# Kernel tuning notes

Hardware: AMD Instinct MI355X
Metric: run time of the kernel (lower is better)

## Reference

```python
import jax, jax.numpy as jnp
import numpy as np

def setup_inputs() -> dict:
    key = jax.random.key(0)
    x = jax.random.normal(key, (4096, 3, 64, 64), dtype=jnp.float32)
    return {"x": x}

def reference(x):
    # x: [N, C=3, H, W]; attention runs over the N dim with feature dim H*W
    N, C, H, W = x.shape
    out = x.reshape(N, C, H * W)          # [N, 3, HW]
    q, k, v = out[:, 0], out[:, 1], out[:, 2]  # each [N, HW]
    dp = (q @ k.T) * 0.5                  # [N, N]
    attn = jax.nn.softmax(dp, axis=-1)
    # dropout omitted (eval-mode / deterministic reference)
    return attn @ v                       # [N, HW]
```

## Files before the change

### kernel.cpp

```cpp
#include <hip/hip_runtime.h>
#include <hip/hip_bf16.h>
#include <cstdint>

#define N 4096
#define ROWSTRIDE 12288

typedef __attribute__((ext_vector_type(8))) _Float16 half8;
typedef __attribute__((ext_vector_type(4))) _Float16 half4v;
typedef __attribute__((ext_vector_type(4))) float floatx4;

__global__ __launch_bounds__(256) void pack_qk(const float* __restrict__ x,
                                               _Float16* __restrict__ qh,
                                               _Float16* __restrict__ kh) {
    const size_t tid = (size_t)blockIdx.x * 256 + threadIdx.x;
    const int i  = (int)(tid >> 10);
    const int c4 = (int)(tid & 1023);
    const float4* xr = (const float4*)(x + (size_t)i * ROWSTRIDE);
    float4 q = xr[c4];
    float4 k = xr[1024 + c4];
    half4v qo = {(_Float16)(q.x * 0.5f), (_Float16)(q.y * 0.5f),
                 (_Float16)(q.z * 0.5f), (_Float16)(q.w * 0.5f)};
    half4v ko = {(_Float16)k.x, (_Float16)k.y, (_Float16)k.z, (_Float16)k.w};
    *(half4v*)(qh + tid * 4) = qo;
    *(half4v*)(kh + tid * 4) = ko;
}

__global__ __launch_bounds__(256) void transpose_v(const float* __restrict__ x,
                                                   _Float16* __restrict__ vt) {
    __shared__ float tile[32][33];
    const int j0 = blockIdx.x * 32;
    const int d0 = blockIdx.y * 32;
    const int t  = threadIdx.x;
    const int r  = t >> 3;
    const int c4 = t & 7;
    const float4 val = *(const float4*)(x + (size_t)(j0 + r) * ROWSTRIDE + 8192 + d0 + c4 * 4);
    tile[r][c4 * 4 + 0] = val.x;
    tile[r][c4 * 4 + 1] = val.y;
    tile[r][c4 * 4 + 2] = val.z;
    tile[r][c4 * 4 + 3] = val.w;
    __syncthreads();
    half4v o = {(_Float16)tile[c4 * 4 + 0][r], (_Float16)tile[c4 * 4 + 1][r],
                (_Float16)tile[c4 * 4 + 2][r], (_Float16)tile[c4 * 4 + 3][r]};
    *(half4v*)(vt + (size_t)(d0 + r) * N + j0 + c4 * 4) = o;
}

#define GL2LDS(g, l)                                                                     \
    __builtin_amdgcn_global_load_lds((const __attribute__((address_space(1))) void*)(g), \
                                     (__attribute__((address_space(3))) void*)(l), 16, 0, 0)

__global__ __launch_bounds__(256) void gemm_nt(const _Float16* __restrict__ A,
                                               const _Float16* __restrict__ Bt,
                                               float* __restrict__ C) {
    __shared__ _Float16 As[2 * 128 * 32];
    __shared__ _Float16 Bs[2 * 128 * 32];
    const int t    = threadIdx.x;
    const int wave = t >> 6;
    const int lane = t & 63;
    const int wr   = wave >> 1, wc = wave & 1;
    const int rowBase = blockIdx.y * 128;
    const int colBase = blockIdx.x * 128;

    floatx4 acc[4][4] = {};

    const int ldRow = t >> 2;
    const int ldCol = (t & 3) * 8;
    const _Float16* ga0 = A  + (size_t)(rowBase + ldRow) * N + ldCol;
    const _Float16* gb0 = Bt + (size_t)(colBase + ldRow) * N + ldCol;
    _Float16* lA = &As[wave * 512];
    _Float16* lB = &Bs[wave * 512];

    const int fr = lane & 15;
    const int fk = (lane >> 4) * 8;

    for (int kt = 0; kt < 64; ++kt) {
        const int k0 = kt * 64;
        __syncthreads();
        GL2LDS(ga0 + k0, lA);
        GL2LDS(ga0 + k0 + (size_t)64 * N, lA + 2048);
        GL2LDS(gb0 + k0, lB);
        GL2LDS(gb0 + k0 + (size_t)64 * N, lB + 2048);
        GL2LDS(ga0 + k0 + 32, lA + 4096);
        GL2LDS(ga0 + k0 + 32 + (size_t)64 * N, lA + 6144);
        GL2LDS(gb0 + k0 + 32, lB + 4096);
        GL2LDS(gb0 + k0 + 32 + (size_t)64 * N, lB + 6144);
        __syncthreads();

#pragma unroll
        for (int ks = 0; ks < 2; ++ks) {
            half8 af[4], bf[4];
#pragma unroll
            for (int mt = 0; mt < 4; ++mt)
                af[mt] = *(half8*)&As[ks * 4096 + (wr * 64 + mt * 16 + fr) * 32 + fk];
#pragma unroll
            for (int nt = 0; nt < 4; ++nt)
                bf[nt] = *(half8*)&Bs[ks * 4096 + (wc * 64 + nt * 16 + fr) * 32 + fk];
#pragma unroll
            for (int mt = 0; mt < 4; ++mt)
#pragma unroll
                for (int nt = 0; nt < 4; ++nt)
                    acc[mt][nt] = __builtin_amdgcn_mfma_f32_16x16x32_f16(af[mt], bf[nt],
                                                                         acc[mt][nt], 0, 0, 0);
        }
    }

    const int quad = lane >> 4;
#pragma unroll
    for (int mt = 0; mt < 4; ++mt) {
#pragma unroll
        for (int nt = 0; nt < 4; ++nt) {
#pragma unroll
            for (int r = 0; r < 4; ++r) {
                const int row = rowBase + wr * 64 + mt * 16 + quad * 4 + r;
                const int col = colBase + wc * 64 + nt * 16 + fr;
                C[(size_t)row * N + col] = acc[mt][nt][r];
            }
        }
    }
}

__global__ __launch_bounds__(256) void softmax_rows(const float* __restrict__ S,
                                                    _Float16* __restrict__ P) {
    const int row = blockIdx.x;
    const int t   = threadIdx.x;
    const float4* Sr = (const float4*)(S + (size_t)row * N);

    float4 v[4];
    float lmax = -3.0e38f;
#pragma unroll
    for (int r = 0; r < 4; ++r) {
        v[r] = Sr[t + 256 * r];
        lmax = fmaxf(lmax, fmaxf(fmaxf(v[r].x, v[r].y), fmaxf(v[r].z, v[r].w)));
    }
#pragma unroll
    for (int off = 32; off; off >>= 1) lmax = fmaxf(lmax, __shfl_xor(lmax, off, 64));
    __shared__ float redm[4], reds[4];
    const int wave = t >> 6, lane = t & 63;
    if (lane == 0) redm[wave] = lmax;
    __syncthreads();
    const float m = fmaxf(fmaxf(redm[0], redm[1]), fmaxf(redm[2], redm[3]));

    float lsum = 0.f;
#pragma unroll
    for (int r = 0; r < 4; ++r) {
        v[r].x = __expf(v[r].x - m);
        v[r].y = __expf(v[r].y - m);
        v[r].z = __expf(v[r].z - m);
        v[r].w = __expf(v[r].w - m);
        lsum += (v[r].x + v[r].y) + (v[r].z + v[r].w);
    }
#pragma unroll
    for (int off = 32; off; off >>= 1) lsum += __shfl_xor(lsum, off, 64);
    if (lane == 0) reds[wave] = lsum;
    __syncthreads();
    const float inv = 1.0f / (((reds[0] + reds[1]) + (reds[2] + reds[3])));

#pragma unroll
    for (int r = 0; r < 4; ++r) {
        half4v o = {(_Float16)(v[r].x * inv), (_Float16)(v[r].y * inv),
                    (_Float16)(v[r].z * inv), (_Float16)(v[r].w * inv)};
        *(half4v*)(P + (size_t)row * N + (t + 256 * r) * 4) = o;
    }
}

extern "C" void kernel_launch(void* const* d_in, const int* in_sizes, int n_in,
                              void* d_out, int out_size, void* d_ws, size_t ws_size,
                              hipStream_t stream) {
    const float* x = (const float*)d_in[0];
    float* out     = (float*)d_out;
    char* ws       = (char*)d_ws;

    _Float16* qh = (_Float16*)(ws);
    _Float16* kh = (_Float16*)(ws + (32ull << 20));
    _Float16* vt = (_Float16*)(ws + (64ull << 20));
    float*    S  = (float*)   (ws + (96ull << 20));
    _Float16* P  = qh;

    pack_qk    <<<16384, 256, 0, stream>>>(x, qh, kh);
    transpose_v<<<dim3(128, 128), 256, 0, stream>>>(x, vt);
    gemm_nt    <<<dim3(32, 32), 256, 0, stream>>>(qh, kh, S);
    softmax_rows<<<4096, 256, 0, stream>>>(S, P);
    gemm_nt    <<<dim3(32, 32), 256, 0, stream>>>(P, vt, out);
}
```

Measured before the change: 629.2 us.

## Replace GEMM with 256x256-tile, 8-wave, double-buffered pipelined kernel

The 128x128 GEMM used for both QK^T and PV is replaced by a 256x256-tile kernel with 512 threads. It double-buffers LDS, interleaves global-to-LDS loads with MFMA work, and uses s_setprio around MFMA bursts. It also applies an XOR swizzle to LDS columns to avoid bank conflicts and remaps workgroup IDs for L2 locality. The aim is to raise MFMA utilization and hide memory latency, at the cost of a full 128KB of LDS per block, more accumulator registers, and fewer blocks on a 4096x4096 problem, which risks a tail effect.

```diff
diff --git a/kernel.cpp b/kernel.cpp
--- a/kernel.cpp
+++ b/kernel.cpp
@@ -48,74 +48,143 @@
     __builtin_amdgcn_global_load_lds((const __attribute__((address_space(1))) void*)(g), \
                                      (__attribute__((address_space(3))) void*)(l), 16, 0, 0)
 
-__global__ __launch_bounds__(256) void gemm_nt(const _Float16* __restrict__ A,
-                                               const _Float16* __restrict__ Bt,
-                                               float* __restrict__ C) {
-    __shared__ _Float16 As[2 * 128 * 32];
-    __shared__ _Float16 Bs[2 * 128 * 32];
+__global__ __launch_bounds__(512, 2) void gemm_nt256(const _Float16* __restrict__ A,
+                                                     const _Float16* __restrict__ Bt,
+                                                     float* __restrict__ C) {
+    __shared__ _Float16 lds[65536];
     const int t    = threadIdx.x;
     const int wave = t >> 6;
     const int lane = t & 63;
-    const int wr   = wave >> 1, wc = wave & 1;
-    const int rowBase = blockIdx.y * 128;
-    const int colBase = blockIdx.x * 128;
-
-    floatx4 acc[4][4] = {};
-
-    const int ldRow = t >> 2;
-    const int ldCol = (t & 3) * 8;
-    const _Float16* ga0 = A  + (size_t)(rowBase + ldRow) * N + ldCol;
-    const _Float16* gb0 = Bt + (size_t)(colBase + ldRow) * N + ldCol;
-    _Float16* lA = &As[wave * 512];
-    _Float16* lB = &Bs[wave * 512];
-
-    const int fr = lane & 15;
-    const int fk = (lane >> 4) * 8;
-
-    for (int kt = 0; kt < 64; ++kt) {
-        const int k0 = kt * 64;
-        __syncthreads();
-        GL2LDS(ga0 + k0, lA);
-        GL2LDS(ga0 + k0 + (size_t)64 * N, lA + 2048);
-        GL2LDS(gb0 + k0, lB);
-        GL2LDS(gb0 + k0 + (size_t)64 * N, lB + 2048);
-        GL2LDS(ga0 + k0 + 32, lA + 4096);
-        GL2LDS(ga0 + k0 + 32 + (size_t)64 * N, lA + 6144);
-        GL2LDS(gb0 + k0 + 32, lB + 4096);
-        GL2LDS(gb0 + k0 + 32 + (size_t)64 * N, lB + 6144);
-        __syncthreads();
-
-#pragma unroll
-        for (int ks = 0; ks < 2; ++ks) {
+    const int wr   = wave >> 2;
+    const int wc   = wave & 3;
+
+    const int orig = blockIdx.y * 16 + blockIdx.x;
+    const int wg   = (orig & 7) * 32 + (orig >> 3);
+    const int rowBase = (wg >> 4) * 256;
+    const int colBase = (wg & 15) * 256;
+
+    floatx4 acc[8][4] = {};
+
+    const int sRow = t >> 2;
+    const int sCg  = (t & 3) ^ ((t >> 3) & 3);
+    const _Float16* gA = A  + (size_t)(rowBase + sRow) * N + sCg * 8;
+    const _Float16* gB = Bt + (size_t)(colBase + sRow) * N + sCg * 8;
+    const int ldsW = wave * 512;
+
+    const int fr   = lane & 15;
+    const int quad = lane >> 4;
+    const int swc  = quad ^ ((fr >> 1) & 3);
+    const int rdA  = (wr * 128 + fr) * 32 + swc * 8;
+    const int rdB  = (wc * 64 + fr) * 32 + swc * 8;
+
+#define STAGE(regOff, g, kOff)                                                  \
+    do {                                                                        \
+        GL2LDS((g) + (kOff), &lds[(regOff) + ldsW]);                            \
+        GL2LDS((g) + (kOff) + (size_t)128 * N, &lds[(regOff) + 4096 + ldsW]);   \
+    } while (0)
+
+    STAGE(0, gA, 0);
+    STAGE(8192, gB, 0);
+    STAGE(16384, gA, 32);
+    STAGE(24576, gB, 32);
+    asm volatile("s_waitcnt vmcnt(4)" ::: "memory");
+    __builtin_amdgcn_s_barrier();
+
+    for (int kt = 0; kt < 63; ++kt) {
+        const int rb = (kt & 1) * 32768;
+        const int sb = rb ^ 32768;
+        const int kNext = (kt + 1) * 64;
+#pragma unroll
+        for (int kh = 0; kh < 2; ++kh) {
+            const int rA = rb + kh * 16384;
+            const int rB = rA + 8192;
             half8 af[4], bf[4];
 #pragma unroll
-            for (int mt = 0; mt < 4; ++mt)
-                af[mt] = *(half8*)&As[ks * 4096 + (wr * 64 + mt * 16 + fr) * 32 + fk];
-#pragma unroll
-            for (int nt = 0; nt < 4; ++nt)
-                bf[nt] = *(half8*)&Bs[ks * 4096 + (wc * 64 + nt * 16 + fr) * 32 + fk];
+            for (int nt = 0; nt < 4; ++nt) bf[nt] = *(const half8*)&lds[rB + nt * 512 + rdB];
+#pragma unroll
+            for (int mt = 0; mt < 4; ++mt) af[mt] = *(const half8*)&lds[rA + mt * 512 + rdA];
+            STAGE(sb + kh * 16384, gA, kNext + kh * 32);
+            __builtin_amdgcn_s_barrier();
+            asm volatile("s_waitcnt lgkmcnt(0)" ::: "memory");
+            __builtin_amdgcn_s_setprio(1);
 #pragma unroll
             for (int mt = 0; mt < 4; ++mt)
 #pragma unroll
                 for (int nt = 0; nt < 4; ++nt)
                     acc[mt][nt] = __builtin_amdgcn_mfma_f32_16x16x32_f16(af[mt], bf[nt],
                                                                          acc[mt][nt], 0, 0, 0);
+            __builtin_amdgcn_s_setprio(0);
+            __builtin_amdgcn_s_barrier();
+#pragma unroll
+            for (int mt = 0; mt < 4; ++mt) af[mt] = *(const half8*)&lds[rA + (mt + 4) * 512 + rdA];
+            STAGE(sb + kh * 16384 + 8192, gB, kNext + kh * 32);
+            asm volatile("s_waitcnt vmcnt(4)" ::: "memory");
+            __builtin_amdgcn_s_barrier();
+            asm volatile("s_waitcnt lgkmcnt(0)" ::: "memory");
+            __builtin_amdgcn_s_setprio(1);
+#pragma unroll
+            for (int mt = 0; mt < 4; ++mt)
+#pragma unroll
+                for (int nt = 0; nt < 4; ++nt)
+                    acc[mt + 4][nt] = __builtin_amdgcn_mfma_f32_16x16x32_f16(af[mt], bf[nt],
+                                                                             acc[mt + 4][nt], 0, 0, 0);
+            __builtin_amdgcn_s_setprio(0);
+            __builtin_amdgcn_s_barrier();
         }
     }
 
-    const int quad = lane >> 4;
-#pragma unroll
-    for (int mt = 0; mt < 4; ++mt) {
+    {
+        const int rb = 32768;
+#pragma unroll
+        for (int kh = 0; kh < 2; ++kh) {
+            const int rA = rb + kh * 16384;
+            const int rB = rA + 8192;
+            half8 af[4], bf[4];
+#pragma unroll
+            for (int nt = 0; nt < 4; ++nt) bf[nt] = *(const half8*)&lds[rB + nt * 512 + rdB];
+#pragma unroll
+            for (int mt = 0; mt < 4; ++mt) af[mt] = *(const half8*)&lds[rA + mt * 512 + rdA];
+            __builtin_amdgcn_s_barrier();
+            asm volatile("s_waitcnt lgkmcnt(0)" ::: "memory");
+            __builtin_amdgcn_s_setprio(1);
+#pragma unroll
+            for (int mt = 0; mt < 4; ++mt)
+#pragma unroll
+                for (int nt = 0; nt < 4; ++nt)
+                    acc[mt][nt] = __builtin_amdgcn_mfma_f32_16x16x32_f16(af[mt], bf[nt],
+                                                                         acc[mt][nt], 0, 0, 0);
+            __builtin_amdgcn_s_setprio(0);
+            __builtin_amdgcn_s_barrier();
+#pragma unroll
+            for (int mt = 0; mt < 4; ++mt) af[mt] = *(const half8*)&lds[rA + (mt + 4) * 512 + rdA];
+            if (kh == 0) asm volatile("s_waitcnt vmcnt(0)" ::: "memory");
+            __builtin_amdgcn_s_barrier();
+            asm volatile("s_waitcnt lgkmcnt(0)" ::: "memory");
+            __builtin_amdgcn_s_setprio(1);
+#pragma unroll
+            for (int mt = 0; mt < 4; ++mt)
+#pragma unroll
+                for (int nt = 0; nt < 4; ++nt)
+                    acc[mt + 4][nt] = __builtin_amdgcn_mfma_f32_16x16x32_f16(af[mt], bf[nt],
+                                                                             acc[mt + 4][nt], 0, 0, 0);
+            __builtin_amdgcn_s_setprio(0);
+            __builtin_amdgcn_s_barrier();
+        }
+    }
+
+#pragma unroll
+    for (int mt = 0; mt < 8; ++mt) {
 #pragma unroll
         for (int nt = 0; nt < 4; ++nt) {
 #pragma unroll
             for (int r = 0; r < 4; ++r) {
-                const int row = rowBase + wr * 64 + mt * 16 + quad * 4 + r;
+                const int row = rowBase + wr * 128 + mt * 16 + quad * 4 + r;
                 const int col = colBase + wc * 64 + nt * 16 + fr;
                 C[(size_t)row * N + col] = acc[mt][nt][r];
             }
         }
     }
+#undef STAGE
 }
 
 __global__ __launch_bounds__(256) void softmax_rows(const float* __restrict__ S,
@@ -175,9 +244,9 @@
     float*    S  = (float*)   (ws + (96ull << 20));
     _Float16* P  = qh;
 
-    pack_qk    <<<16384, 256, 0, stream>>>(x, qh, kh);
-    transpose_v<<<dim3(128, 128), 256, 0, stream>>>(x, vt);
-    gemm_nt    <<<dim3(32, 32), 256, 0, stream>>>(qh, kh, S);
+    pack_qk     <<<16384, 256, 0, stream>>>(x, qh, kh);
+    transpose_v <<<dim3(128, 128), 256, 0, stream>>>(x, vt);
+    gemm_nt256  <<<dim3(16, 16), 512, 0, stream>>>(qh, kh, S);
     softmax_rows<<<4096, 256, 0, stream>>>(S, P);
-    gemm_nt    <<<dim3(32, 32), 256, 0, stream>>>(P, vt, out);
-}
+    gemm_nt256  <<<dim3(16, 16), 512, 0, stream>>>(P, vt, out);
+}
```

Result: faster. 546.7 us (-13.1%).
